# Kernel tuning notes

Measured on AMD Instinct MI355X. Metric: run time of the kernel, lower is better.

Reference implementation:

```python
import jax, jax.numpy as jnp
import numpy as np

COST_CLS, COST_MASK, COST_DICE = 2.0, 5.0, 5.0


def setup_inputs() -> dict:
    key = jax.random.key(0)
    k1, k2, k3, k4 = jax.random.split(key, 4)
    B, Q, C, H, W, T, Hg, Wg = 4, 100, 81, 256, 256, 20, 512, 512
    pred_logits = jax.random.normal(k1, (B, Q, C), dtype=jnp.float32)
    pred_masks = jax.random.normal(k2, (B, Q, H, W), dtype=jnp.float32)
    # binary GT instance masks (original uses 0/1 masks)
    tgt_masks = (jax.random.uniform(k3, (B, T, Hg, Wg)) < 0.5).astype(jnp.float32)
    tgt_labels = jax.random.randint(k4, (B, T), 0, C).astype(jnp.int64)
    return {"pred_logits": pred_logits, "pred_masks": pred_masks,
            "tgt_masks": tgt_masks, "tgt_labels": tgt_labels}


def _cost_matrices(pred_logits, pred_masks, tgt_masks, tgt_labels):
    # pred_logits [B,Q,C], pred_masks [B,Q,H,W], tgt_masks [B,T,Hg,Wg], tgt_labels [B,T]
    B, Q, H, W = pred_masks.shape
    T, Hg, Wg = tgt_masks.shape[1:]
    # F.interpolate(mode='nearest') down to pred mask size: src = floor(dst * in/out)
    ri = (jnp.arange(H) * Hg) // H
    ci = (jnp.arange(W) * Wg) // W
    tgt = tgt_masks[:, :, ri][:, :, :, ci]          # [B,T,H,W]
    pm = pred_masks.reshape(B, Q, H * W)            # [B,Q,HW]
    tm = tgt.reshape(B, T, H * W)                   # [B,T,HW]
    hw = float(H * W)
    # classification cost: -softmax(logits)[:, tgt_ids]
    prob = jax.nn.softmax(pred_logits, axis=-1)     # [B,Q,C]
    cost_class = -jnp.take_along_axis(prob, tgt_labels[:, None, :], axis=2)  # [B,Q,T]
    # batch_sigmoid_ce_loss: mean over pixels of BCE-with-logits vs 0/1 target
    pos = jax.nn.softplus(-pm)                      # -log sigmoid(x)
    neg = jax.nn.softplus(pm)                       # -log (1 - sigmoid(x))
    cost_mask = (jnp.einsum('bqp,btp->bqt', pos, tm)
                 + jnp.einsum('bqp,btp->bqt', neg, 1.0 - tm)) / hw
    # batch_dice_loss
    sig = jax.nn.sigmoid(pm)
    numer = 2.0 * jnp.einsum('bqp,btp->bqt', sig, tm)
    denom = sig.sum(-1)[:, :, None] + tm.sum(-1)[:, None, :]
    cost_dice = 1.0 - (numer + 1.0) / (denom + 1.0)
    C = COST_CLS * cost_class + COST_MASK * cost_mask + COST_DICE * cost_dice
    return jnp.nan_to_num(C, nan=0.0)               # [B,Q,T]


_cost_jit = jax.jit(_cost_matrices)


def _lsa(cost):
    """Shortest-augmenting-path linear sum assignment (scipy algorithm).
    cost: (R, Cn) numpy array with R <= Cn. Returns col4row[r] = assigned column."""
    R, Cn = cost.shape
    u = np.zeros(R, dtype=np.float64)
    v = np.zeros(Cn, dtype=np.float64)
    col4row = np.full(R, -1, dtype=np.int64)
    row4col = np.full(Cn, -1, dtype=np.int64)
    cost = cost.astype(np.float64)
    for cur_row in range(R):
        shortest = np.full(Cn, np.inf)
        path = np.full(Cn, -1, dtype=np.int64)
        SR = np.zeros(R, dtype=bool)
        SC = np.zeros(Cn, dtype=bool)
        i = cur_row
        minVal = 0.0
        sink = -1
        while sink == -1:
            SR[i] = True
            rem = np.where(~SC)[0]
            d = minVal + cost[i, rem] - u[i] - v[rem]
            upd = d < shortest[rem]
            shortest[rem[upd]] = d[upd]
            path[rem[upd]] = i
            jloc = rem[np.argmin(shortest[rem])]
            minVal = shortest[jloc]
            SC[jloc] = True
            if row4col[jloc] == -1:
                sink = jloc
            else:
                i = row4col[jloc]
        u[cur_row] += minVal
        mask = SR.copy(); mask[cur_row] = False
        u[mask] += minVal - shortest[col4row[mask]]
        v[SC] -= minVal - shortest[SC]
        j = sink
        while True:
            i = path[j]
            row4col[j] = i
            col4row[i], j = j, col4row[i]
            if i == cur_row:
                break
    return col4row


def reference(pred_logits, pred_masks, tgt_masks, tgt_labels):
    C = _cost_jit(pred_logits, pred_masks, tgt_masks, tgt_labels)  # [B,Q,T]
    Cn = np.asarray(C)
    B, Q, T = Cn.shape
    pred_idx, tgt_idx = [], []
    for b in range(B):
        # solve on the transpose (T <= Q): target t -> query q[t]
        q = _lsa(Cn[b].T)
        t = np.arange(T)
        order = np.argsort(q)  # scipy returns row (query) indices in sorted order
        pred_idx.append(q[order])
        tgt_idx.append(t[order])
    return (C,
            jnp.asarray(np.stack(pred_idx), dtype=jnp.int64),
            jnp.asarray(np.stack(tgt_idx), dtype=jnp.int64))
```

## Files before the change

### kernel.cpp

```cpp
#include <hip/hip_runtime.h>
#include <hip/hip_bf16.h>
#include <math.h>
#include <stdint.h>

#define NB 4
#define NQ 100
#define NQR 101
#define NCLS 81
#define NT 20
#define NHW 65536

#define SC 256
#define CPX (NHW / SC)
#define TP 32

typedef __attribute__((ext_vector_type(8))) short bf16x8;
typedef __attribute__((ext_vector_type(16))) float f32x16;

__device__ inline short to_bf16(float f) {
    __hip_bfloat16 h = __float2bfloat16(f);
    return __builtin_bit_cast(short, h);
}

__device__ inline float fast_exp2(float x) { return __builtin_amdgcn_exp2f(x); }
__device__ inline float fast_log2(float x) { return __builtin_amdgcn_logf(x); }

__global__ void __launch_bounds__(256)
k_main(const float* __restrict__ pm, const float* __restrict__ tgt,
       float* __restrict__ A_part, float* __restrict__ D_part,
       float* __restrict__ Sp_part) {
    int gid = blockIdx.x;
    int chunk = gid & (SC - 1);
    int b = gid >> 8;
    int tid = threadIdx.x;
    int wv = tid >> 6, lane = tid & 63;
    int p0 = chunk * CPX;

    __shared__ uint32_t s_tb[CPX];
    __shared__ float s_pm[128 * 64];
    __shared__ short s_bf[4][512];

    if (tid < 128) {
        const float* base = tgt + (((size_t)b * NT) * 512 + 2 * chunk) * 512 + 4 * tid;
        uint32_t w0 = 0, w1 = 0;
#pragma unroll
        for (int t = 0; t < NT; ++t) {
            float4 v = *reinterpret_cast<const float4*>(base + (size_t)t * 512 * 512);
            w0 |= (v.x > 0.5f ? 1u : 0u) << t;
            w1 |= (v.z > 0.5f ? 1u : 0u) << t;
        }
        s_tb[2 * tid] = w0;
        s_tb[2 * tid + 1] = w1;
    }
    __syncthreads();

    int r0 = tid >> 4, cw = tid & 15;
    int Rg = wv * 32 + (lane & 31);
    int h = lane >> 5;
    const bool ones_row = (Rg == NQ);
    bf16x8 ones;
#pragma unroll
    for (int e = 0; e < 8; ++e) ones[e] = (short)0x3F80;

    f32x16 accA, accD;
#pragma unroll
    for (int r = 0; r < 16; ++r) { accA[r] = 0.0f; accD[r] = 0.0f; }
    float mxsum = 0.0f, l2sum = 0.0f;
    const float LOG2E = 1.4426950408889634f;

    for (int st = 0; st < 4; ++st) {
        {
            int ls = wv;
            int col = lane & 31;
            int kbase = st * 64 + ls * 16 + (h << 3);
            uint32_t pk[4];
#pragma unroll
            for (int e2 = 0; e2 < 4; ++e2) {
                uint32_t w0 = s_tb[kbase + 2 * e2];
                uint32_t w1 = s_tb[kbase + 2 * e2 + 1];
                uint32_t lo, hi;
                if (col < NT)       { lo = ((w0 >> col) & 1u) ? 0x3F80u : 0u;
                                      hi = ((w1 >> col) & 1u) ? 0x3F80u : 0u; }
                else if (col == NT) { lo = 0x3F80u; hi = 0x3F80u; }
                else                { lo = 0u; hi = 0u; }
                pk[e2] = lo | (hi << 16);
            }
            *reinterpret_cast<uint4*>(&s_bf[ls][lane * 8]) =
                *reinterpret_cast<const uint4*>(pk);
        }
#pragma unroll
        for (int p = 0; p < 8; ++p) {
            int row = r0 + 16 * p;
            int srow = (row < NQ) ? row : 0;
            float4 v = *reinterpret_cast<const float4*>(
                pm + ((size_t)(b * NQ + srow)) * NHW + (p0 + st * 64 + cw * 4));
            *reinterpret_cast<float4*>(
                &s_pm[row * 64 + ((cw ^ (row & 7)) << 2)]) = v;
        }
        __syncthreads();
#pragma unroll
        for (int sl = 0; sl < 4; ++sl) {
            int c0 = sl * 4 + h * 2;
            float4 xa = *reinterpret_cast<const float4*>(
                &s_pm[Rg * 64 + ((c0 ^ (Rg & 7)) << 2)]);
            float4 xb4 = *reinterpret_cast<const float4*>(
                &s_pm[Rg * 64 + (((c0 + 1) ^ (Rg & 7)) << 2)]);
            float xs[8] = {xa.x, xa.y, xa.z, xa.w, xb4.x, xb4.y, xb4.z, xb4.w};
            bf16x8 af, sf;
#pragma unroll
            for (int e = 0; e < 8; ++e) {
                float xi = xs[e];
                float y = xi * LOG2E;
                float e1 = fast_exp2(0.0f - fabsf(y));
                float tt = 1.0f + e1;
                float inv = __builtin_amdgcn_rcpf(tt);
                float sig = (xi >= 0.0f) ? inv : e1 * inv;
                l2sum += fast_log2(tt);
                mxsum += fmaxf(xi, 0.0f);
                af[e] = to_bf16(xi);
                sf[e] = to_bf16(sig);
            }
            if (ones_row) af = ones;
            bf16x8 bf = *reinterpret_cast<const bf16x8*>(&s_bf[sl][lane * 8]);
            accA = __builtin_amdgcn_mfma_f32_32x32x16_bf16(af, bf, accA, 0, 0, 0);
            accD = __builtin_amdgcn_mfma_f32_32x32x16_bf16(sf, bf, accD, 0, 0, 0);
        }
        __syncthreads();
    }

    int t = lane & 31;
#pragma unroll
    for (int r = 0; r < 16; ++r) {
        int rowD = (r & 3) + 8 * (r >> 2) + 4 * (lane >> 5);
        int qo = wv * 32 + rowD;
        if (qo <= NQ && t <= NT) {
            size_t base = ((size_t)(b * NQR + qo) * SC + chunk) * TP + t;
            A_part[base] = accA[r];
            D_part[base] = accD[r];
        }
    }
    float sp = fmaf(0.6931471805599453f, l2sum, mxsum);
    sp += __shfl_xor(sp, 32);
    if (lane < 32 && Rg < NQ)
        Sp_part[(size_t)(b * NQ + Rg) * SC + chunk] = sp;
}

__global__ void __launch_bounds__(256)
k_assemble(const float* __restrict__ logits, const int* __restrict__ labels,
           const float* __restrict__ A_part, const float* __restrict__ D_part,
           const float* __restrict__ Sp_part, float* __restrict__ Cout) {
    int bq = blockIdx.x;
    int q = bq % NQ, b = bq / NQ;
    int tid = threadIdx.x, wv = tid >> 6, lane = tid & 63;
    int t = tid & 31, g = tid >> 5;
    __shared__ float sA[4][32], sD[4][32], sS[4][32], sSn[4];

    const float* pa = A_part + (size_t)(b * NQR + q) * SC * TP;
    const float* pd = D_part + (size_t)(b * NQR + q) * SC * TP;
    const float* ps = A_part + (size_t)(b * NQR + NQ) * SC * TP;
    const float* pp = Sp_part + (size_t)(b * NQ + q) * SC;

    float a = 0.0f, d = 0.0f, s = 0.0f;
    for (int c = g; c < SC; c += 8) {
        a += pa[c * TP + t];
        d += pd[c * TP + t];
        s += ps[c * TP + t];
    }
    a += __shfl_xor(a, 32);
    d += __shfl_xor(d, 32);
    s += __shfl_xor(s, 32);
    if (lane < 32) { sA[wv][lane] = a; sD[wv][lane] = d; sS[wv][lane] = s; }
    {
        float sp = pp[tid & 255 & (SC - 1)];
        for (int o = 32; o; o >>= 1) sp += __shfl_xor(sp, o);
        if (lane == 0) sSn[wv] = sp;
    }
    __syncthreads();

    if (wv == 0) {
        int lt = (lane < 32) ? lane : 0;
        float At4 = sA[0][lt] + sA[1][lt] + sA[2][lt] + sA[3][lt];
        float Dt4 = sD[0][lt] + sD[1][lt] + sD[2][lt] + sD[3][lt];
        float St4 = sS[0][lt] + sS[1][lt] + sS[2][lt] + sS[3][lt];
        float Sneg = sSn[0] + sSn[1] + sSn[2] + sSn[3];
        float Ssig = __shfl(Dt4, NT);

        const float* lg = logits + (size_t)bq * NCLS;
        float x0 = (lane < NCLS) ? lg[lane] : -INFINITY;
        float x1 = (lane + 64 < NCLS) ? lg[lane + 64] : -INFINITY;
        float mx = fmaxf(x0, x1);
        for (int o = 32; o; o >>= 1) mx = fmaxf(mx, __shfl_xor(mx, o));
        float s0 = (lane < NCLS) ? __expf(x0 - mx) : 0.0f;
        float s1 = (lane + 64 < NCLS) ? __expf(x1 - mx) : 0.0f;
        float sum = s0 + s1;
        for (int o = 32; o; o >>= 1) sum += __shfl_xor(sum, o);

        if (lane < NT) {
            int label = labels[b * NT + lane];
            float prob = __expf(lg[label] - mx) / sum;
            float cm = (Sneg - At4) * (1.0f / (float)NHW);
            float cd = 1.0f - (2.0f * Dt4 + 1.0f) / (Ssig + St4 + 1.0f);
            float c = 2.0f * (-prob) + 5.0f * cm + 5.0f * cd;
            if (isnan(c)) c = 0.0f;
            Cout[(size_t)bq * NT + lane] = c;
        }
    }
}

__global__ void __launch_bounds__(64)
k_lsa(const float* __restrict__ Cmat, float* __restrict__ out) {
    int b = blockIdx.x;
    int lane = threadIdx.x;
    __shared__ double s_cost[NT][128];

    for (int idx = lane; idx < NT * 128; idx += 64) {
        int r = idx >> 7, j = idx & 127;
        s_cost[r][j] = (j < NQ) ? (double)Cmat[((size_t)b * NQ + j) * NT + r] : 0.0;
    }
    __syncthreads();

    int j0 = lane, j1 = lane + 64;
    bool v1ok = (j1 < NQ);
    double v_0 = 0.0, v_1 = 0.0;
    int r4c0 = -1, r4c1 = -1;
    double u_r = 0.0;
    int c4r = -1;

    for (int cur = 0; cur < NT; ++cur) {
        double sh0 = INFINITY, sh1 = INFINITY;
        int p0 = -1, p1 = -1;
        bool sc0 = false, sc1 = false;
        bool SRr = false;
        int i = cur, sink = -1;
        double minVal = 0.0;

        while (true) {
            if (lane == i) SRr = true;
            double ui = __shfl(u_r, i);
            double c0 = s_cost[i][j0];
            double c1 = s_cost[i][j1 & 127];
            if (!sc0) {
                double d = (minVal + c0 - ui) - v_0;
                if (d < sh0) { sh0 = d; p0 = i; }
            }
            if (v1ok && !sc1) {
                double d = (minVal + c1 - ui) - v_1;
                if (d < sh1) { sh1 = d; p1 = i; }
            }
            double cand0 = (!sc0) ? sh0 : INFINITY;
            double cand1 = (v1ok && !sc1) ? sh1 : INFINITY;
            double bv; int bj;
            if (cand0 <= cand1) { bv = cand0; bj = j0; }
            else                { bv = cand1; bj = j1; }
            for (int o = 32; o; o >>= 1) {
                double ov = __shfl_xor(bv, o);
                int oj = __shfl_xor(bj, o);
                if (ov < bv || (ov == bv && oj < bj)) { bv = ov; bj = oj; }
            }
            minVal = bv;
            if (bj < 64) { if (lane == bj) sc0 = true; }
            else         { if (lane == bj - 64) sc1 = true; }
            int r4 = (bj < 64) ? __shfl(r4c0, bj) : __shfl(r4c1, bj - 64);
            if (r4 == -1) { sink = bj; break; }
            i = r4;
        }

        {
            int c = c4r;
            double g0 = __shfl(sh0, c & 63);
            double g1 = __shfl(sh1, (c - 64) & 63);
            double shc = (c < 64) ? g0 : g1;
            if (lane == cur) u_r += minVal;
            else if (lane < NT && SRr) u_r += minVal - shc;
        }
        if (sc0) v_0 -= minVal - sh0;
        if (v1ok && sc1) v_1 -= minVal - sh1;

        int j = sink;
        while (true) {
            int ii = (j < 64) ? __shfl(p0, j) : __shfl(p1, j - 64);
            if (j < 64) { if (lane == j) r4c0 = ii; }
            else        { if (lane == j - 64) r4c1 = ii; }
            int nj = __shfl(c4r, ii);
            if (lane == ii) c4r = j;
            if (ii == cur) break;
            j = nj;
        }
    }

    int my = c4r;
    int rank = 0;
#pragma unroll
    for (int t2 = 0; t2 < NT; ++t2) {
        int vv = __shfl(my, t2);
        rank += (vv < my) ? 1 : 0;
    }
    if (lane < NT) {
        out[NB * NQ * NT + b * NT + rank] = (float)my;
        out[NB * NQ * NT + NB * NT + b * NT + rank] = (float)lane;
    }
}

extern "C" void kernel_launch(void* const* d_in, const int* in_sizes, int n_in,
                              void* d_out, int out_size, void* d_ws, size_t ws_size,
                              hipStream_t stream) {
    const float* pred_logits = (const float*)d_in[0];
    const float* pred_masks  = (const float*)d_in[1];
    const float* tgt_masks   = (const float*)d_in[2];
    const int*   tgt_labels  = (const int*)d_in[3];
    float* out = (float*)d_out;

    char* ws = (char*)d_ws;
    float* A_part  = (float*)ws;
    float* D_part  = A_part + (size_t)NB * NQR * SC * TP;
    float* Sp_part = D_part + (size_t)NB * NQR * SC * TP;

    k_main<<<NB * SC, 256, 0, stream>>>(pred_masks, tgt_masks, A_part, D_part, Sp_part);
    k_assemble<<<NB * NQ, 256, 0, stream>>>(pred_logits, tgt_labels, A_part, D_part,
                                            Sp_part, out);
    k_lsa<<<NB, 64, 0, stream>>>(out, out);
}
```

Before: 79.65 us.

## Stage pred masks as bf16 in LDS and split pixels into more chunks

Pred-mask tiles are converted to bf16 at load time and stored in a smaller swizzled LDS buffer holding only the 101 needed rows instead of 128 padded fp32 rows. The main kernel is templated on the chunk count and uses 512 pixel chunks when the workspace is large enough, doubling the grid for more parallelism. The trade-off is larger partial buffers for the assemble kernel to reduce. Softplus and sigmoid are now computed from bf16-rounded inputs, which loosens precision slightly.

```diff
diff --git a/kernel.cpp b/kernel.cpp
--- a/kernel.cpp
+++ b/kernel.cpp
@@ -9,9 +9,6 @@
 #define NCLS 81
 #define NT 20
 #define NHW 65536
-
-#define SC 256
-#define CPX (NHW / SC)
 #define TP 32
 
 typedef __attribute__((ext_vector_type(8))) short bf16x8;
@@ -21,27 +18,34 @@
     __hip_bfloat16 h = __float2bfloat16(f);
     return __builtin_bit_cast(short, h);
 }
-
+__device__ inline float from_bf16(short s) {
+    return __builtin_bit_cast(float, ((uint32_t)(uint16_t)s) << 16);
+}
 __device__ inline float fast_exp2(float x) { return __builtin_amdgcn_exp2f(x); }
 __device__ inline float fast_log2(float x) { return __builtin_amdgcn_logf(x); }
 
+template<int SCv>
 __global__ void __launch_bounds__(256)
 k_main(const float* __restrict__ pm, const float* __restrict__ tgt,
        float* __restrict__ A_part, float* __restrict__ D_part,
        float* __restrict__ Sp_part) {
+    constexpr int CPXv = NHW / SCv;
+    constexpr int NST = CPXv / 64;
     int gid = blockIdx.x;
-    int chunk = gid & (SC - 1);
-    int b = gid >> 8;
+    int chunk = gid & (SCv - 1);
+    int b = gid / SCv;
     int tid = threadIdx.x;
     int wv = tid >> 6, lane = tid & 63;
-    int p0 = chunk * CPX;
-
-    __shared__ uint32_t s_tb[CPX];
-    __shared__ float s_pm[128 * 64];
+    int p0 = chunk * CPXv;
+
+    __shared__ uint32_t s_tb[CPXv];
+    __shared__ short s_pm[101 * 64];
     __shared__ short s_bf[4][512];
 
-    if (tid < 128) {
-        const float* base = tgt + (((size_t)b * NT) * 512 + 2 * chunk) * 512 + 4 * tid;
+    if (tid < CPXv / 2) {
+        int hrow = p0 >> 8, pc0 = p0 & 255;
+        const float* base = tgt + (((size_t)b * NT) * 512 + 2 * hrow) * 512
+                                + 2 * pc0 + 4 * tid;
         uint32_t w0 = 0, w1 = 0;
 #pragma unroll
         for (int t = 0; t < NT; ++t) {
@@ -54,9 +58,10 @@
     }
     __syncthreads();
 
-    int r0 = tid >> 4, cw = tid & 15;
     int Rg = wv * 32 + (lane & 31);
+    int rcl = (Rg < 101) ? Rg : 0;
     int h = lane >> 5;
+    int col = lane & 31;
     const bool ones_row = (Rg == NQ);
     bf16x8 ones;
 #pragma unroll
@@ -68,11 +73,9 @@
     float mxsum = 0.0f, l2sum = 0.0f;
     const float LOG2E = 1.4426950408889634f;
 
-    for (int st = 0; st < 4; ++st) {
+    for (int st = 0; st < NST; ++st) {
         {
-            int ls = wv;
-            int col = lane & 31;
-            int kbase = st * 64 + ls * 16 + (h << 3);
+            int kbase = st * 64 + wv * 16 + (h << 3);
             uint32_t pk[4];
 #pragma unroll
             for (int e2 = 0; e2 < 4; ++e2) {
@@ -85,31 +88,37 @@
                 else                { lo = 0u; hi = 0u; }
                 pk[e2] = lo | (hi << 16);
             }
-            *reinterpret_cast<uint4*>(&s_bf[ls][lane * 8]) =
+            *reinterpret_cast<uint4*>(&s_bf[wv][lane * 8]) =
                 *reinterpret_cast<const uint4*>(pk);
         }
-#pragma unroll
-        for (int p = 0; p < 8; ++p) {
-            int row = r0 + 16 * p;
-            int srow = (row < NQ) ? row : 0;
-            float4 v = *reinterpret_cast<const float4*>(
-                pm + ((size_t)(b * NQ + srow)) * NHW + (p0 + st * 64 + cw * 4));
-            *reinterpret_cast<float4*>(
-                &s_pm[row * 64 + ((cw ^ (row & 7)) << 2)]) = v;
+        for (int ch = tid; ch < 800; ch += 256) {
+            int row = ch >> 3, cw = ch & 7;
+            int sw = cw ^ (row & 7);
+            const float* g = pm + ((size_t)(b * NQ + row)) * NHW
+                                + (p0 + st * 64 + sw * 8);
+            float4 f0 = *reinterpret_cast<const float4*>(g);
+            float4 f1 = *reinterpret_cast<const float4*>(g + 4);
+            uint32_t q0 = (uint32_t)(uint16_t)to_bf16(f0.x)
+                        | ((uint32_t)(uint16_t)to_bf16(f0.y) << 16);
+            uint32_t q1 = (uint32_t)(uint16_t)to_bf16(f0.z)
+                        | ((uint32_t)(uint16_t)to_bf16(f0.w) << 16);
+            uint32_t q2 = (uint32_t)(uint16_t)to_bf16(f1.x)
+                        | ((uint32_t)(uint16_t)to_bf16(f1.y) << 16);
+            uint32_t q3 = (uint32_t)(uint16_t)to_bf16(f1.z)
+                        | ((uint32_t)(uint16_t)to_bf16(f1.w) << 16);
+            uint4 pkw = make_uint4(q0, q1, q2, q3);
+            *reinterpret_cast<uint4*>(&s_pm[row * 64 + cw * 8]) = pkw;
         }
         __syncthreads();
 #pragma unroll
         for (int sl = 0; sl < 4; ++sl) {
-            int c0 = sl * 4 + h * 2;
-            float4 xa = *reinterpret_cast<const float4*>(
-                &s_pm[Rg * 64 + ((c0 ^ (Rg & 7)) << 2)]);
-            float4 xb4 = *reinterpret_cast<const float4*>(
-                &s_pm[Rg * 64 + (((c0 + 1) ^ (Rg & 7)) << 2)]);
-            float xs[8] = {xa.x, xa.y, xa.z, xa.w, xb4.x, xb4.y, xb4.z, xb4.w};
-            bf16x8 af, sf;
+            int c = sl * 2 + h;
+            bf16x8 af = *reinterpret_cast<const bf16x8*>(
+                &s_pm[rcl * 64 + ((c ^ (rcl & 7)) << 3)]);
+            bf16x8 sf;
 #pragma unroll
             for (int e = 0; e < 8; ++e) {
-                float xi = xs[e];
+                float xi = from_bf16(af[e]);
                 float y = xi * LOG2E;
                 float e1 = fast_exp2(0.0f - fabsf(y));
                 float tt = 1.0f + e1;
@@ -117,7 +126,6 @@
                 float sig = (xi >= 0.0f) ? inv : e1 * inv;
                 l2sum += fast_log2(tt);
                 mxsum += fmaxf(xi, 0.0f);
-                af[e] = to_bf16(xi);
                 sf[e] = to_bf16(sig);
             }
             if (ones_row) af = ones;
@@ -134,7 +142,7 @@
         int rowD = (r & 3) + 8 * (r >> 2) + 4 * (lane >> 5);
         int qo = wv * 32 + rowD;
         if (qo <= NQ && t <= NT) {
-            size_t base = ((size_t)(b * NQR + qo) * SC + chunk) * TP + t;
+            size_t base = ((size_t)(b * NQR + qo) * SCv + chunk) * TP + t;
             A_part[base] = accA[r];
             D_part[base] = accD[r];
         }
@@ -142,9 +150,10 @@
     float sp = fmaf(0.6931471805599453f, l2sum, mxsum);
     sp += __shfl_xor(sp, 32);
     if (lane < 32 && Rg < NQ)
-        Sp_part[(size_t)(b * NQ + Rg) * SC + chunk] = sp;
-}
-
+        Sp_part[(size_t)(b * NQ + Rg) * SCv + chunk] = sp;
+}
+
+template<int SCv>
 __global__ void __launch_bounds__(256)
 k_assemble(const float* __restrict__ logits, const int* __restrict__ labels,
            const float* __restrict__ A_part, const float* __restrict__ D_part,
@@ -155,13 +164,13 @@
     int t = tid & 31, g = tid >> 5;
     __shared__ float sA[4][32], sD[4][32], sS[4][32], sSn[4];
 
-    const float* pa = A_part + (size_t)(b * NQR + q) * SC * TP;
-    const float* pd = D_part + (size_t)(b * NQR + q) * SC * TP;
-    const float* ps = A_part + (size_t)(b * NQR + NQ) * SC * TP;
-    const float* pp = Sp_part + (size_t)(b * NQ + q) * SC;
+    const float* pa = A_part + (size_t)(b * NQR + q) * SCv * TP;
+    const float* pd = D_part + (size_t)(b * NQR + q) * SCv * TP;
+    const float* ps = A_part + (size_t)(b * NQR + NQ) * SCv * TP;
+    const float* pp = Sp_part + (size_t)(b * NQ + q) * SCv;
 
     float a = 0.0f, d = 0.0f, s = 0.0f;
-    for (int c = g; c < SC; c += 8) {
+    for (int c = g; c < SCv; c += 8) {
         a += pa[c * TP + t];
         d += pd[c * TP + t];
         s += ps[c * TP + t];
@@ -171,7 +180,8 @@
     s += __shfl_xor(s, 32);
     if (lane < 32) { sA[wv][lane] = a; sD[wv][lane] = d; sS[wv][lane] = s; }
     {
-        float sp = pp[tid & 255 & (SC - 1)];
+        float sp = 0.0f;
+        for (int i = tid; i < SCv; i += 256) sp += pp[i];
         for (int o = 32; o; o >>= 1) sp += __shfl_xor(sp, o);
         if (lane == 0) sSn[wv] = sp;
     }
@@ -309,14 +319,28 @@
     const float* tgt_masks   = (const float*)d_in[2];
     const int*   tgt_labels  = (const int*)d_in[3];
     float* out = (float*)d_out;
-
     char* ws = (char*)d_ws;
-    float* A_part  = (float*)ws;
-    float* D_part  = A_part + (size_t)NB * NQR * SC * TP;
-    float* Sp_part = D_part + (size_t)NB * NQR * SC * TP;
-
-    k_main<<<NB * SC, 256, 0, stream>>>(pred_masks, tgt_masks, A_part, D_part, Sp_part);
-    k_assemble<<<NB * NQ, 256, 0, stream>>>(pred_logits, tgt_labels, A_part, D_part,
-                                            Sp_part, out);
+
+    const size_t need512 = 2ull * NB * NQR * 512 * TP * 4 + (size_t)NB * NQ * 512 * 4;
+
+    if (ws_size >= need512) {
+        constexpr int SCv = 512;
+        float* A_part  = (float*)ws;
+        float* D_part  = A_part + (size_t)NB * NQR * SCv * TP;
+        float* Sp_part = D_part + (size_t)NB * NQR * SCv * TP;
+        k_main<SCv><<<NB * SCv, 256, 0, stream>>>(pred_masks, tgt_masks,
+                                                  A_part, D_part, Sp_part);
+        k_assemble<SCv><<<NB * NQ, 256, 0, stream>>>(pred_logits, tgt_labels,
+                                                     A_part, D_part, Sp_part, out);
+    } else {
+        constexpr int SCv = 256;
+        float* A_part  = (float*)ws;
+        float* D_part  = A_part + (size_t)NB * NQR * SCv * TP;
+        float* Sp_part = D_part + (size_t)NB * NQR * SCv * TP;
+        k_main<SCv><<<NB * SCv, 256, 0, stream>>>(pred_masks, tgt_masks,
+                                                  A_part, D_part, Sp_part);
+        k_assemble<SCv><<<NB * NQ, 256, 0, stream>>>(pred_logits, tgt_labels,
+                                                     A_part, D_part, Sp_part, out);
+    }
     k_lsa<<<NB, 64, 0, stream>>>(out, out);
 }
```

New measurement: 97.85 us. +22.9%, slower.
